# Kernel tuning notes

Measured on AMD Instinct MI355X. Metric: run time of the kernel, lower is better.

The kernel has to match this reference:

```python
import jax, jax.numpy as jnp
import numpy as np

N = 4096      # num_nodes
F = 256       # node_dim
K = 4         # num_heads
FP = 64       # out_dim per head
P_EDGE = 0.008  # edge probability (~33 avg degree)


def setup_inputs() -> dict:
    key = jax.random.key(0)
    k1, k2, k3, k4, k5 = jax.random.split(key, 5)
    x = jax.random.normal(k1, (N, F), dtype=jnp.float32)
    # binary adjacency mask with self loops so every row has a neighbor
    adj = (jax.random.uniform(k2, (N, N)) < P_EDGE).astype(jnp.float32)
    mask = jnp.maximum(adj, jnp.eye(N, dtype=jnp.float32))
    batch = jnp.zeros((N,), dtype=jnp.int32)  # unused (is_final_layer=False)
    # xavier-style init for W (node_dim -> K*FP) and attention vectors
    w_scale = np.sqrt(2.0 / (F + K * FP)).astype(np.float32)
    W = jax.random.normal(k3, (F, K * FP), dtype=jnp.float32) * w_scale
    b = jnp.zeros((K * FP,), dtype=jnp.float32)
    a_scale = np.sqrt(2.0 / (K * FP + 1)).astype(np.float32)
    a_left = jax.random.normal(k4, (1, K, FP), dtype=jnp.float32) * a_scale
    a_right = jax.random.normal(k5, (1, K, FP), dtype=jnp.float32) * a_scale
    return {"x": x, "mask": mask, "batch": batch, "W": W, "b": b,
            "a_left": a_left, "a_right": a_right}


def reference(x, mask, batch, W, b, a_left, a_right):
    # dropout prob = 0.0 (eval mode) -> identity
    x_proj = (x @ W + b).reshape(N, K, FP)                 # (N,K,F')
    score_src = (x_proj * a_left).sum(axis=-1)             # (N,K)
    score_tgt = (x_proj * a_right).sum(axis=-1)            # (N,K)
    score = score_src[:, None, :] + score_tgt[None, :, :]  # (N,N,K)
    score = jax.nn.leaky_relu(score, negative_slope=0.2)
    # non-standard global mean/std normalization (torch .std() is unbiased)
    score = (score - score.mean()) / score.std(ddof=1)
    score = jnp.exp(score)
    m = mask[:, :, None]                                   # (N,N,1)
    denom = (score * m).sum(axis=1, keepdims=True)         # (N,1,K)
    aij = (score / denom) * m                              # (N,N,K)
    attention = jnp.transpose(aij, (2, 0, 1))              # (K,N,N)
    h_prime = jnp.einsum('knm,mkf->nkf', attention, x_proj)  # (N,K,F')
    h_prime = jax.nn.elu(h_prime)
    # is_final_layer=False -> concat heads
    return h_prime.reshape(N, K * FP)
```

## Files before the change

kernel.cpp:

```cpp
#include <hip/hip_runtime.h>
#include <hip/hip_bf16.h>
#include <math.h>

#define NN 4096
#define FF 256
#define KH 4
#define FP 64
#define NCOL 256
#define MAXNBR 512
#define GEMM_BLKS 512
#define MOM_BLOCKS 1024
#define MOM_ROWS 4

__device__ __forceinline__ float bits2f(unsigned b) {
    union { unsigned u; float f; } c; c.u = b << 16; return c.f;
}
__device__ __forceinline__ int is_fp32(const void* mask) {
    return ((const unsigned*)mask)[0] == 0x3F800000u;
}

#define OFF_PART   0
#define OFF_MUSIG  65536
#define OFF_XP     131072
#define OFF_SRC    4325376
#define OFF_TGT    4390912
#define OFF_NBR    4456448
#define OFF_CNT    8650752

__global__ __launch_bounds__(256) void k_gemm_scan(
        const void* __restrict__ xr, const void* __restrict__ mask,
        const void* __restrict__ Wr, const void* __restrict__ br,
        const void* __restrict__ alr, const void* __restrict__ arr,
        float* __restrict__ xp, float* __restrict__ srcb, float* __restrict__ tgtb,
        unsigned short* __restrict__ nbr_g, int* __restrict__ cnt_g) {
    const int fl = is_fp32(mask);
    const int tid = threadIdx.x;
    __shared__ union {
        float4 xs[8][64];
        struct { unsigned short snbr[MAXNBR]; int cnt; } sc;
    } sm;

    if (blockIdx.x >= GEMM_BLKS) {
        int n = blockIdx.x - GEMM_BLKS;
        if (tid == 0) sm.sc.cnt = 0;
        __syncthreads();
        if (fl) {
            const uint4* p = (const uint4*)((const float*)mask + (size_t)n * NN);
            for (int i = tid; i < NN / 4; i += 256) {
                uint4 v = p[i]; int base = i * 4;
                if (v.x) { int s = atomicAdd(&sm.sc.cnt, 1); if (s < MAXNBR) sm.sc.snbr[s] = base + 0; }
                if (v.y) { int s = atomicAdd(&sm.sc.cnt, 1); if (s < MAXNBR) sm.sc.snbr[s] = base + 1; }
                if (v.z) { int s = atomicAdd(&sm.sc.cnt, 1); if (s < MAXNBR) sm.sc.snbr[s] = base + 2; }
                if (v.w) { int s = atomicAdd(&sm.sc.cnt, 1); if (s < MAXNBR) sm.sc.snbr[s] = base + 3; }
            }
        } else {
            const uint4* p = (const uint4*)((const unsigned short*)mask + (size_t)n * NN);
            for (int i = tid; i < NN / 8; i += 256) {
                uint4 v = p[i]; int base = i * 8;
                if (v.x & 0xFFFFu) { int s = atomicAdd(&sm.sc.cnt, 1); if (s < MAXNBR) sm.sc.snbr[s] = base + 0; }
                if (v.x >> 16)     { int s = atomicAdd(&sm.sc.cnt, 1); if (s < MAXNBR) sm.sc.snbr[s] = base + 1; }
                if (v.y & 0xFFFFu) { int s = atomicAdd(&sm.sc.cnt, 1); if (s < MAXNBR) sm.sc.snbr[s] = base + 2; }
                if (v.y >> 16)     { int s = atomicAdd(&sm.sc.cnt, 1); if (s < MAXNBR) sm.sc.snbr[s] = base + 3; }
                if (v.z & 0xFFFFu) { int s = atomicAdd(&sm.sc.cnt, 1); if (s < MAXNBR) sm.sc.snbr[s] = base + 4; }
                if (v.z >> 16)     { int s = atomicAdd(&sm.sc.cnt, 1); if (s < MAXNBR) sm.sc.snbr[s] = base + 5; }
                if (v.w & 0xFFFFu) { int s = atomicAdd(&sm.sc.cnt, 1); if (s < MAXNBR) sm.sc.snbr[s] = base + 6; }
                if (v.w >> 16)     { int s = atomicAdd(&sm.sc.cnt, 1); if (s < MAXNBR) sm.sc.snbr[s] = base + 7; }
            }
        }
        __syncthreads();
        int c = sm.sc.cnt < MAXNBR ? sm.sc.cnt : MAXNBR;
        for (int j = tid; j < c; j += 256)
            nbr_g[(size_t)n * MAXNBR + j] = sm.sc.snbr[j];
        if (tid == 0) cnt_g[n] = c;
        return;
    }

    int n0 = blockIdx.x * 8;
    if (fl) {
        const float4* xq = (const float4*)xr;
        for (int t = tid; t < 512; t += 256) {
            int r = t >> 6, q = t & 63;
            sm.xs[r][q] = xq[(size_t)(n0 + r) * 64 + q];
        }
    } else {
        const ushort4* xq = (const ushort4*)xr;
        for (int t = tid; t < 512; t += 256) {
            int r = t >> 6, q = t & 63;
            ushort4 u = xq[(size_t)(n0 + r) * 64 + q];
            float4 v; v.x = bits2f(u.x); v.y = bits2f(u.y); v.z = bits2f(u.z); v.w = bits2f(u.w);
            sm.xs[r][q] = v;
        }
    }
    __syncthreads();
    int c = tid;
    float acc[8] = {};
    if (fl) {
        const float* WF = (const float*)Wr;
        for (int kk = 0; kk < 64; ++kk) {
            float w0 = WF[(4 * kk + 0) * NCOL + c];
            float w1 = WF[(4 * kk + 1) * NCOL + c];
            float w2 = WF[(4 * kk + 2) * NCOL + c];
            float w3 = WF[(4 * kk + 3) * NCOL + c];
            #pragma unroll
            for (int r = 0; r < 8; ++r) {
                float4 xv = sm.xs[r][kk];
                acc[r] += xv.x * w0 + xv.y * w1 + xv.z * w2 + xv.w * w3;
            }
        }
    } else {
        const unsigned short* WB = (const unsigned short*)Wr;
        for (int kk = 0; kk < 64; ++kk) {
            float w0 = bits2f(WB[(4 * kk + 0) * NCOL + c]);
            float w1 = bits2f(WB[(4 * kk + 1) * NCOL + c]);
            float w2 = bits2f(WB[(4 * kk + 2) * NCOL + c]);
            float w3 = bits2f(WB[(4 * kk + 3) * NCOL + c]);
            #pragma unroll
            for (int r = 0; r < 8; ++r) {
                float4 xv = sm.xs[r][kk];
                acc[r] += xv.x * w0 + xv.y * w1 + xv.z * w2 + xv.w * w3;
            }
        }
    }
    float bv, alv, arv;
    if (fl) {
        bv  = ((const float*)br)[c];
        alv = ((const float*)alr)[c];
        arv = ((const float*)arr)[c];
    } else {
        bv  = bits2f(((const unsigned short*)br)[c]);
        alv = bits2f(((const unsigned short*)alr)[c]);
        arv = bits2f(((const unsigned short*)arr)[c]);
    }
    int wave = tid >> 6;
    int lane = tid & 63;
    #pragma unroll
    for (int r = 0; r < 8; ++r) {
        float o = acc[r] + bv;
        xp[(size_t)(n0 + r) * NCOL + c] = o;
        float sr = o * alv, tr = o * arv;
        #pragma unroll
        for (int off = 32; off; off >>= 1) {
            sr += __shfl_down(sr, off, 64);
            tr += __shfl_down(tr, off, 64);
        }
        if (lane == 0) {
            srcb[(n0 + r) * KH + wave] = sr;
            tgtb[(n0 + r) * KH + wave] = tr;
        }
    }
}

__global__ __launch_bounds__(256) void k_moments(
        const float* __restrict__ srcb, const float* __restrict__ tgtb,
        double2* __restrict__ partials) {
    const int tid = threadIdx.x;
    const int n0 = blockIdx.x * MOM_ROWS;
    const float4* s4 = (const float4*)srcb;
    float4 sv0 = s4[n0 + 0], sv1 = s4[n0 + 1], sv2 = s4[n0 + 2], sv3 = s4[n0 + 3];
    float a1_0 = 0.f, a2_0 = 0.f, a1_1 = 0.f, a2_1 = 0.f;
    float a1_2 = 0.f, a2_2 = 0.f, a1_3 = 0.f, a2_3 = 0.f;
    #pragma unroll 2
    for (int m = tid; m < NN; m += 256) {
        float4 tv = ((const float4*)tgtb)[m];
        #define MROW(sv, A1, A2) { \
            float v0 = sv.x + tv.x; v0 = fmaxf(v0, 0.2f * v0); \
            float v1 = sv.y + tv.y; v1 = fmaxf(v1, 0.2f * v1); \
            float v2 = sv.z + tv.z; v2 = fmaxf(v2, 0.2f * v2); \
            float v3 = sv.w + tv.w; v3 = fmaxf(v3, 0.2f * v3); \
            A1 += (v0 + v1) + (v2 + v3); \
            A2 += (v0 * v0 + v1 * v1) + (v2 * v2 + v3 * v3); }
        MROW(sv0, a1_0, a2_0)
        MROW(sv1, a1_1, a2_1)
        MROW(sv2, a1_2, a2_2)
        MROW(sv3, a1_3, a2_3)
        #undef MROW
    }
    __shared__ double l1[256], l2[256];
    l1[tid] = ((double)a1_0 + (double)a1_1) + ((double)a1_2 + (double)a1_3);
    l2[tid] = ((double)a2_0 + (double)a2_1) + ((double)a2_2 + (double)a2_3);
    __syncthreads();
    for (int off = 128; off; off >>= 1) {
        if (tid < off) {
            l1[tid] += l1[tid + off];
            l2[tid] += l2[tid + off];
        }
        __syncthreads();
    }
    if (tid == 0) {
        double2 pr; pr.x = l1[0]; pr.y = l2[0];
        partials[blockIdx.x] = pr;
    }
}

__global__ __launch_bounds__(256) void k_fold(
        const double2* __restrict__ partials, float* __restrict__ musig) {
    double a = 0.0, b2 = 0.0;
    for (int i = threadIdx.x; i < MOM_BLOCKS; i += 256) {
        double2 pr = partials[i];
        a += pr.x; b2 += pr.y;
    }
    __shared__ double l1[256], l2[256];
    l1[threadIdx.x] = a;
    l2[threadIdx.x] = b2;
    __syncthreads();
    for (int off = 128; off; off >>= 1) {
        if (threadIdx.x < off) {
            l1[threadIdx.x] += l1[threadIdx.x + off];
            l2[threadIdx.x] += l2[threadIdx.x + off];
        }
        __syncthreads();
    }
    if (threadIdx.x == 0) {
        double s = l1[0], ss = l2[0];
        const double tot = (double)NN * (double)NN * (double)KH;
        musig[0] = (float)(s / tot);
        musig[1] = (float)(1.0 / sqrt((ss - s * s / tot) / (tot - 1.0)));
    }
}

__global__ __launch_bounds__(256) void k_aggregate(
        const unsigned short* __restrict__ nbr_g, const int* __restrict__ cnt_g,
        const float* __restrict__ musig,
        const float* __restrict__ xp,
        const float* __restrict__ srcb, const float* __restrict__ tgtb,
        float* __restrict__ out) {
    const int tid = threadIdx.x;
    const int wave = tid >> 6, lane = tid & 63;
    __shared__ unsigned short snbr[MAXNBR];
    __shared__ float pls[MAXNBR * KH];
    __shared__ float invden[KH];
    __shared__ float4 red[4][64];
    float mu = musig[0], inv_sigma = musig[1];
    int n = blockIdx.x;
    int c = cnt_g[n];
    for (int j = tid; j < c; j += 256) snbr[j] = nbr_g[(size_t)n * MAXNBR + j];
    __syncthreads();

    for (int t = tid; t < c * KH; t += 256) {
        int j = t >> 2, k = t & 3;
        int m = snbr[j];
        float v = srcb[n * KH + k] + tgtb[m * KH + k];
        v = v > 0.f ? v : 0.2f * v;
        pls[t] = expf((v - mu) * inv_sigma);
    }
    __syncthreads();

    {
        float d = 0.f;
        for (int j = lane; j < c; j += 64) d += pls[j * KH + wave];
        #pragma unroll
        for (int off = 32; off; off >>= 1) d += __shfl_down(d, off, 64);
        if (lane == 0) invden[wave] = 1.0f / d;
    }
    __syncthreads();

    const int k = lane >> 4;
    const float4* xp4 = (const float4*)xp;
    float4 acc = make_float4(0.f, 0.f, 0.f, 0.f);
    int j = wave;
    for (; j + 4 < c; j += 8) {
        int m0 = snbr[j], m1 = snbr[j + 4];
        float w0 = pls[j * KH + k], w1 = pls[(j + 4) * KH + k];
        float4 a = xp4[(size_t)m0 * 64 + lane];
        float4 b = xp4[(size_t)m1 * 64 + lane];
        acc.x += w0 * a.x + w1 * b.x;
        acc.y += w0 * a.y + w1 * b.y;
        acc.z += w0 * a.z + w1 * b.z;
        acc.w += w0 * a.w + w1 * b.w;
    }
    if (j < c) {
        int m0 = snbr[j];
        float w0 = pls[j * KH + k];
        float4 a = xp4[(size_t)m0 * 64 + lane];
        acc.x += w0 * a.x; acc.y += w0 * a.y;
        acc.z += w0 * a.z; acc.w += w0 * a.w;
    }
    red[wave][lane] = acc;
    __syncthreads();
    if (tid < 64) {
        float4 r0 = red[0][tid], r1 = red[1][tid], r2 = red[2][tid], r3 = red[3][tid];
        float s = invden[tid >> 4];
        float4 o;
        o.x = (r0.x + r1.x + r2.x + r3.x) * s;
        o.y = (r0.y + r1.y + r2.y + r3.y) * s;
        o.z = (r0.z + r1.z + r2.z + r3.z) * s;
        o.w = (r0.w + r1.w + r2.w + r3.w) * s;
        o.x = o.x > 0.f ? o.x : expm1f(o.x);
        o.y = o.y > 0.f ? o.y : expm1f(o.y);
        o.z = o.z > 0.f ? o.z : expm1f(o.z);
        o.w = o.w > 0.f ? o.w : expm1f(o.w);
        ((float4*)out)[(size_t)n * 64 + tid] = o;
    }
}

extern "C" void kernel_launch(void* const* d_in, const int* in_sizes, int n_in,
                              void* d_out, int out_size, void* d_ws, size_t ws_size,
                              hipStream_t stream) {
    const void* x    = d_in[0];
    const void* mask = d_in[1];
    const void* W    = d_in[3];
    const void* b    = d_in[4];
    const void* al   = d_in[5];
    const void* ar   = d_in[6];

    char* ws = (char*)d_ws;
    double2* part = (double2*)(ws + OFF_PART);
    float* musig = (float*)(ws + OFF_MUSIG);
    float* xp   = (float*)(ws + OFF_XP);
    float* src  = (float*)(ws + OFF_SRC);
    float* tgt  = (float*)(ws + OFF_TGT);
    unsigned short* nbr = (unsigned short*)(ws + OFF_NBR);
    int* cntg = (int*)(ws + OFF_CNT);

    k_gemm_scan<<<GEMM_BLKS + NN, 256, 0, stream>>>(x, mask, W, b, al, ar,
                                                    xp, src, tgt, nbr, cntg);
    k_moments<<<MOM_BLOCKS, 256, 0, stream>>>(src, tgt, part);
    k_fold<<<1, 256, 0, stream>>>(part, musig);
    k_aggregate<<<NN, 256, 0, stream>>>(nbr, cntg, musig, xp, src, tgt,
                                        (float*)d_out);
}
```

Baseline: 147.4 us.

## Fuse mask scan and moment fold into aggregate kernel, drop separate launches

Moves the per-row adjacency scan out of the GEMM kernel and into the aggregate kernel, so neighbor lists are built in shared memory and no longer written to or read back from global memory. Folds the 1024 moment partials redundantly in every aggregate block, which removes the single-block fold kernel and one launch. The cost is that each of the 4096 aggregate blocks now rereads 16KB of partials and does a double-precision tree reduction, and the 64MB mask scan now sits on the critical path of the aggregate kernel instead of running alongside the GEMM.

Measured after the change: 150.6 us. 2.2% more time.

```diff
diff --git a/kernel.cpp b/kernel.cpp
--- a/kernel.cpp
+++ b/kernel.cpp
@@ -20,67 +20,25 @@
 }
 
 #define OFF_PART   0
-#define OFF_MUSIG  65536
 #define OFF_XP     131072
 #define OFF_SRC    4325376
 #define OFF_TGT    4390912
-#define OFF_NBR    4456448
-#define OFF_CNT    8650752
-
-__global__ __launch_bounds__(256) void k_gemm_scan(
+
+__global__ __launch_bounds__(256) void k_gemm(
         const void* __restrict__ xr, const void* __restrict__ mask,
         const void* __restrict__ Wr, const void* __restrict__ br,
         const void* __restrict__ alr, const void* __restrict__ arr,
-        float* __restrict__ xp, float* __restrict__ srcb, float* __restrict__ tgtb,
-        unsigned short* __restrict__ nbr_g, int* __restrict__ cnt_g) {
+        float* __restrict__ xp, float* __restrict__ srcb, float* __restrict__ tgtb) {
     const int fl = is_fp32(mask);
     const int tid = threadIdx.x;
-    __shared__ union {
-        float4 xs[8][64];
-        struct { unsigned short snbr[MAXNBR]; int cnt; } sc;
-    } sm;
-
-    if (blockIdx.x >= GEMM_BLKS) {
-        int n = blockIdx.x - GEMM_BLKS;
-        if (tid == 0) sm.sc.cnt = 0;
-        __syncthreads();
-        if (fl) {
-            const uint4* p = (const uint4*)((const float*)mask + (size_t)n * NN);
-            for (int i = tid; i < NN / 4; i += 256) {
-                uint4 v = p[i]; int base = i * 4;
-                if (v.x) { int s = atomicAdd(&sm.sc.cnt, 1); if (s < MAXNBR) sm.sc.snbr[s] = base + 0; }
-                if (v.y) { int s = atomicAdd(&sm.sc.cnt, 1); if (s < MAXNBR) sm.sc.snbr[s] = base + 1; }
-                if (v.z) { int s = atomicAdd(&sm.sc.cnt, 1); if (s < MAXNBR) sm.sc.snbr[s] = base + 2; }
-                if (v.w) { int s = atomicAdd(&sm.sc.cnt, 1); if (s < MAXNBR) sm.sc.snbr[s] = base + 3; }
-            }
-        } else {
-            const uint4* p = (const uint4*)((const unsigned short*)mask + (size_t)n * NN);
-            for (int i = tid; i < NN / 8; i += 256) {
-                uint4 v = p[i]; int base = i * 8;
-                if (v.x & 0xFFFFu) { int s = atomicAdd(&sm.sc.cnt, 1); if (s < MAXNBR) sm.sc.snbr[s] = base + 0; }
-                if (v.x >> 16)     { int s = atomicAdd(&sm.sc.cnt, 1); if (s < MAXNBR) sm.sc.snbr[s] = base + 1; }
-                if (v.y & 0xFFFFu) { int s = atomicAdd(&sm.sc.cnt, 1); if (s < MAXNBR) sm.sc.snbr[s] = base + 2; }
-                if (v.y >> 16)     { int s = atomicAdd(&sm.sc.cnt, 1); if (s < MAXNBR) sm.sc.snbr[s] = base + 3; }
-                if (v.z & 0xFFFFu) { int s = atomicAdd(&sm.sc.cnt, 1); if (s < MAXNBR) sm.sc.snbr[s] = base + 4; }
-                if (v.z >> 16)     { int s = atomicAdd(&sm.sc.cnt, 1); if (s < MAXNBR) sm.sc.snbr[s] = base + 5; }
-                if (v.w & 0xFFFFu) { int s = atomicAdd(&sm.sc.cnt, 1); if (s < MAXNBR) sm.sc.snbr[s] = base + 6; }
-                if (v.w >> 16)     { int s = atomicAdd(&sm.sc.cnt, 1); if (s < MAXNBR) sm.sc.snbr[s] = base + 7; }
-            }
-        }
-        __syncthreads();
-        int c = sm.sc.cnt < MAXNBR ? sm.sc.cnt : MAXNBR;
-        for (int j = tid; j < c; j += 256)
-            nbr_g[(size_t)n * MAXNBR + j] = sm.sc.snbr[j];
-        if (tid == 0) cnt_g[n] = c;
-        return;
-    }
+    __shared__ float4 xs[8][64];
 
     int n0 = blockIdx.x * 8;
     if (fl) {
         const float4* xq = (const float4*)xr;
         for (int t = tid; t < 512; t += 256) {
             int r = t >> 6, q = t & 63;
-            sm.xs[r][q] = xq[(size_t)(n0 + r) * 64 + q];
+            xs[r][q] = xq[(size_t)(n0 + r) * 64 + q];
         }
     } else {
         const ushort4* xq = (const ushort4*)xr;
@@ -88,7 +46,7 @@
             int r = t >> 6, q = t & 63;
             ushort4 u = xq[(size_t)(n0 + r) * 64 + q];
             float4 v; v.x = bits2f(u.x); v.y = bits2f(u.y); v.z = bits2f(u.z); v.w = bits2f(u.w);
-            sm.xs[r][q] = v;
+            xs[r][q] = v;
         }
     }
     __syncthreads();
@@ -103,7 +61,7 @@
             float w3 = WF[(4 * kk + 3) * NCOL + c];
             #pragma unroll
             for (int r = 0; r < 8; ++r) {
-                float4 xv = sm.xs[r][kk];
+                float4 xv = xs[r][kk];
                 acc[r] += xv.x * w0 + xv.y * w1 + xv.z * w2 + xv.w * w3;
             }
         }
@@ -116,7 +74,7 @@
             float w3 = bits2f(WB[(4 * kk + 3) * NCOL + c]);
             #pragma unroll
             for (int r = 0; r < 8; ++r) {
-                float4 xv = sm.xs[r][kk];
+                float4 xv = xs[r][kk];
                 acc[r] += xv.x * w0 + xv.y * w1 + xv.z * w2 + xv.w * w3;
             }
         }
@@ -192,49 +150,78 @@
     }
 }
 
-__global__ __launch_bounds__(256) void k_fold(
-        const double2* __restrict__ partials, float* __restrict__ musig) {
-    double a = 0.0, b2 = 0.0;
-    for (int i = threadIdx.x; i < MOM_BLOCKS; i += 256) {
-        double2 pr = partials[i];
-        a += pr.x; b2 += pr.y;
-    }
-    __shared__ double l1[256], l2[256];
-    l1[threadIdx.x] = a;
-    l2[threadIdx.x] = b2;
-    __syncthreads();
-    for (int off = 128; off; off >>= 1) {
-        if (threadIdx.x < off) {
-            l1[threadIdx.x] += l1[threadIdx.x + off];
-            l2[threadIdx.x] += l2[threadIdx.x + off];
-        }
-        __syncthreads();
-    }
-    if (threadIdx.x == 0) {
-        double s = l1[0], ss = l2[0];
-        const double tot = (double)NN * (double)NN * (double)KH;
-        musig[0] = (float)(s / tot);
-        musig[1] = (float)(1.0 / sqrt((ss - s * s / tot) / (tot - 1.0)));
-    }
-}
-
 __global__ __launch_bounds__(256) void k_aggregate(
-        const unsigned short* __restrict__ nbr_g, const int* __restrict__ cnt_g,
-        const float* __restrict__ musig,
+        const void* __restrict__ mask,
+        const double2* __restrict__ partials,
         const float* __restrict__ xp,
         const float* __restrict__ srcb, const float* __restrict__ tgtb,
         float* __restrict__ out) {
+    const int fl = is_fp32(mask);
     const int tid = threadIdx.x;
     const int wave = tid >> 6, lane = tid & 63;
     __shared__ unsigned short snbr[MAXNBR];
+    __shared__ int scnt;
     __shared__ float pls[MAXNBR * KH];
     __shared__ float invden[KH];
-    __shared__ float4 red[4][64];
-    float mu = musig[0], inv_sigma = musig[1];
-    int n = blockIdx.x;
-    int c = cnt_g[n];
-    for (int j = tid; j < c; j += 256) snbr[j] = nbr_g[(size_t)n * MAXNBR + j];
-    __syncthreads();
+    __shared__ float musig_s[2];
+    __shared__ union {
+        double fold[2][256];
+        float4 red[4][64];
+    } u;
+    const int n = blockIdx.x;
+    if (tid == 0) scnt = 0;
+    __syncthreads();
+
+    if (fl) {
+        const uint4* p = (const uint4*)((const float*)mask + (size_t)n * NN);
+        for (int i = tid; i < NN / 4; i += 256) {
+            uint4 v = p[i]; int base = i * 4;
+            if (v.x) { int s = atomicAdd(&scnt, 1); if (s < MAXNBR) snbr[s] = base + 0; }
+            if (v.y) { int s = atomicAdd(&scnt, 1); if (s < MAXNBR) snbr[s] = base + 1; }
+            if (v.z) { int s = atomicAdd(&scnt, 1); if (s < MAXNBR) snbr[s] = base + 2; }
+            if (v.w) { int s = atomicAdd(&scnt, 1); if (s < MAXNBR) snbr[s] = base + 3; }
+        }
+    } else {
+        const uint4* p = (const uint4*)((const unsigned short*)mask + (size_t)n * NN);
+        for (int i = tid; i < NN / 8; i += 256) {
+            uint4 v = p[i]; int base = i * 8;
+            if (v.x & 0xFFFFu) { int s = atomicAdd(&scnt, 1); if (s < MAXNBR) snbr[s] = base + 0; }
+            if (v.x >> 16)     { int s = atomicAdd(&scnt, 1); if (s < MAXNBR) snbr[s] = base + 1; }
+            if (v.y & 0xFFFFu) { int s = atomicAdd(&scnt, 1); if (s < MAXNBR) snbr[s] = base + 2; }
+            if (v.y >> 16)     { int s = atomicAdd(&scnt, 1); if (s < MAXNBR) snbr[s] = base + 3; }
+            if (v.z & 0xFFFFu) { int s = atomicAdd(&scnt, 1); if (s < MAXNBR) snbr[s] = base + 4; }
+            if (v.z >> 16)     { int s = atomicAdd(&scnt, 1); if (s < MAXNBR) snbr[s] = base + 5; }
+            if (v.w & 0xFFFFu) { int s = atomicAdd(&scnt, 1); if (s < MAXNBR) snbr[s] = base + 6; }
+            if (v.w >> 16)     { int s = atomicAdd(&scnt, 1); if (s < MAXNBR) snbr[s] = base + 7; }
+        }
+    }
+
+    {
+        double a = 0.0, b2 = 0.0;
+        for (int i = tid; i < MOM_BLOCKS; i += 256) {
+            double2 pr = partials[i];
+            a += pr.x; b2 += pr.y;
+        }
+        u.fold[0][tid] = a;
+        u.fold[1][tid] = b2;
+        __syncthreads();
+        for (int off = 128; off; off >>= 1) {
+            if (tid < off) {
+                u.fold[0][tid] += u.fold[0][tid + off];
+                u.fold[1][tid] += u.fold[1][tid + off];
+            }
+            __syncthreads();
+        }
+        if (tid == 0) {
+            double s = u.fold[0][0], ss = u.fold[1][0];
+            const double tot = (double)NN * (double)NN * (double)KH;
+            musig_s[0] = (float)(s / tot);
+            musig_s[1] = (float)(1.0 / sqrt((ss - s * s / tot) / (tot - 1.0)));
+        }
+        __syncthreads();
+    }
+    const float mu = musig_s[0], inv_sigma = musig_s[1];
+    const int c = scnt < MAXNBR ? scnt : MAXNBR;
 
     for (int t = tid; t < c * KH; t += 256) {
         int j = t >> 2, k = t & 3;
@@ -275,10 +262,10 @@
         acc.x += w0 * a.x; acc.y += w0 * a.y;
         acc.z += w0 * a.z; acc.w += w0 * a.w;
     }
-    red[wave][lane] = acc;
+    u.red[wave][lane] = acc;
     __syncthreads();
     if (tid < 64) {
-        float4 r0 = red[0][tid], r1 = red[1][tid], r2 = red[2][tid], r3 = red[3][tid];
+        float4 r0 = u.red[0][tid], r1 = u.red[1][tid], r2 = u.red[2][tid], r3 = u.red[3][tid];
         float s = invden[tid >> 4];
         float4 o;
         o.x = (r0.x + r1.x + r2.x + r3.x) * s;
@@ -305,17 +292,11 @@
 
     char* ws = (char*)d_ws;
     double2* part = (double2*)(ws + OFF_PART);
-    float* musig = (float*)(ws + OFF_MUSIG);
     float* xp   = (float*)(ws + OFF_XP);
     float* src  = (float*)(ws + OFF_SRC);
     float* tgt  = (float*)(ws + OFF_TGT);
-    unsigned short* nbr = (unsigned short*)(ws + OFF_NBR);
-    int* cntg = (int*)(ws + OFF_CNT);
-
-    k_gemm_scan<<<GEMM_BLKS + NN, 256, 0, stream>>>(x, mask, W, b, al, ar,
-                                                    xp, src, tgt, nbr, cntg);
+
+    k_gemm<<<GEMM_BLKS, 256, 0, stream>>>(x, mask, W, b, al, ar, xp, src, tgt);
     k_moments<<<MOM_BLOCKS, 256, 0, stream>>>(src, tgt, part);
-    k_fold<<<1, 256, 0, stream>>>(part, musig);
-    k_aggregate<<<NN, 256, 0, stream>>>(nbr, cntg, musig, xp, src, tgt,
-                                        (float*)d_out);
-}
+    k_aggregate<<<NN, 256, 0, stream>>>(mask, part, xp, src, tgt, (float*)d_out);
+}
```

## Compute attention scores via folded W·a vectors and fuse moments into scan/GEMM kernel

Applied to the files above, without the earlier changes.

Adds a small kernel that folds the attention vectors into W (W·a_left, W·a_right, plus bias terms) so per-node scores come directly from x without waiting on the full projection. This lets the moments reduction run in the same launch as the mask scan and the projection GEMM instead of after it, removing a dependent kernel boundary. The cost is an extra small serial kernel in front that recomputes the folded weights in every block. Summing in a different order also changes the floating-point rounding of the scores.

New measurement: 193.2 us. 1.31x slower.

```diff
diff --git a/kernel.cpp b/kernel.cpp
--- a/kernel.cpp
+++ b/kernel.cpp
@@ -8,6 +8,7 @@
 #define FP 64
 #define NCOL 256
 #define MAXNBR 512
+#define SCAN_BLKS 4096
 #define GEMM_BLKS 512
 #define MOM_BLOCKS 1024
 #define MOM_ROWS 4
@@ -27,21 +28,98 @@
 #define OFF_NBR    4456448
 #define OFF_CNT    8650752
 
-__global__ __launch_bounds__(256) void k_gemm_scan(
+__global__ __launch_bounds__(256) void k_scores(
         const void* __restrict__ xr, const void* __restrict__ mask,
         const void* __restrict__ Wr, const void* __restrict__ br,
         const void* __restrict__ alr, const void* __restrict__ arr,
-        float* __restrict__ xp, float* __restrict__ srcb, float* __restrict__ tgtb,
-        unsigned short* __restrict__ nbr_g, int* __restrict__ cnt_g) {
+        float* __restrict__ srcb, float* __restrict__ tgtb) {
+    const int fl = is_fp32(mask);
+    const int tid = threadIdx.x;
+    __shared__ float al_s[NCOL], ar_s[NCOL];
+    __shared__ float wl_s[FF][KH], wr_s[FF][KH];
+    __shared__ float bl_s[KH], brr_s[KH];
+
+    if (fl) {
+        al_s[tid] = ((const float*)alr)[tid];
+        ar_s[tid] = ((const float*)arr)[tid];
+    } else {
+        al_s[tid] = bits2f(((const unsigned short*)alr)[tid]);
+        ar_s[tid] = bits2f(((const unsigned short*)arr)[tid]);
+    }
+    __syncthreads();
+
+    if (tid < 8) {
+        int k = tid & 3, which = tid >> 2;
+        float s = 0.f;
+        for (int f = 0; f < FP; ++f) {
+            int cc = k * FP + f;
+            float bvv = fl ? ((const float*)br)[cc]
+                           : bits2f(((const unsigned short*)br)[cc]);
+            s += bvv * (which ? ar_s[cc] : al_s[cc]);
+        }
+        if (which) brr_s[k] = s; else bl_s[k] = s;
+    }
+
+    {
+        const float* WrowF = (const float*)Wr + (size_t)tid * NCOL;
+        const unsigned short* WrowB = (const unsigned short*)Wr + (size_t)tid * NCOL;
+        #pragma unroll
+        for (int k = 0; k < KH; ++k) {
+            float sl = 0.f, sr = 0.f;
+            for (int f = 0; f < FP; ++f) {
+                int cc = k * FP + f;
+                float w = fl ? WrowF[cc] : bits2f(WrowB[cc]);
+                sl += w * al_s[cc];
+                sr += w * ar_s[cc];
+            }
+            wl_s[tid][k] = sl;
+            wr_s[tid][k] = sr;
+        }
+    }
+    __syncthreads();
+
+    const int r = tid & 63, k = tid >> 6;
+    const int n = blockIdx.x * 64 + r;
+    float sl = bl_s[k], sr = brr_s[k];
+    if (fl) {
+        const float4* xrow = (const float4*)((const float*)xr + (size_t)n * FF);
+        for (int j4 = 0; j4 < FF / 4; ++j4) {
+            float4 xv = xrow[j4];
+            int j = j4 * 4;
+            sl += xv.x * wl_s[j][k] + xv.y * wl_s[j+1][k] + xv.z * wl_s[j+2][k] + xv.w * wl_s[j+3][k];
+            sr += xv.x * wr_s[j][k] + xv.y * wr_s[j+1][k] + xv.z * wr_s[j+2][k] + xv.w * wr_s[j+3][k];
+        }
+    } else {
+        const ushort4* xrow = (const ushort4*)((const unsigned short*)xr + (size_t)n * FF);
+        for (int j4 = 0; j4 < FF / 4; ++j4) {
+            ushort4 u = xrow[j4];
+            float x0 = bits2f(u.x), x1 = bits2f(u.y), x2 = bits2f(u.z), x3 = bits2f(u.w);
+            int j = j4 * 4;
+            sl += x0 * wl_s[j][k] + x1 * wl_s[j+1][k] + x2 * wl_s[j+2][k] + x3 * wl_s[j+3][k];
+            sr += x0 * wr_s[j][k] + x1 * wr_s[j+1][k] + x2 * wr_s[j+2][k] + x3 * wr_s[j+3][k];
+        }
+    }
+    srcb[n * KH + k] = sl;
+    tgtb[n * KH + k] = sr;
+}
+
+__global__ __launch_bounds__(256) void k_fused(
+        const void* __restrict__ xr, const void* __restrict__ mask,
+        const void* __restrict__ Wr, const void* __restrict__ br,
+        float* __restrict__ xp,
+        const float* __restrict__ srcb, const float* __restrict__ tgtb,
+        unsigned short* __restrict__ nbr_g, int* __restrict__ cnt_g,
+        double2* __restrict__ partials) {
     const int fl = is_fp32(mask);
     const int tid = threadIdx.x;
     __shared__ union {
         float4 xs[8][64];
         struct { unsigned short snbr[MAXNBR]; int cnt; } sc;
+        struct { double l1[256], l2[256]; } mo;
     } sm;
 
-    if (blockIdx.x >= GEMM_BLKS) {
-        int n = blockIdx.x - GEMM_BLKS;
+    if (blockIdx.x < SCAN_BLKS) {
+        int n = blockIdx.x;
         if (tid == 0) sm.sc.cnt = 0;
         __syncthreads();
         if (fl) {
@@ -75,7 +153,46 @@
         return;
     }
 
-    int n0 = blockIdx.x * 8;
+    if (blockIdx.x >= SCAN_BLKS + GEMM_BLKS) {
+        const int n0 = (blockIdx.x - SCAN_BLKS - GEMM_BLKS) * MOM_ROWS;
+        const float4* s4 = (const float4*)srcb;
+        float4 sv0 = s4[n0 + 0], sv1 = s4[n0 + 1], sv2 = s4[n0 + 2], sv3 = s4[n0 + 3];
+        float a1_0 = 0.f, a2_0 = 0.f, a1_1 = 0.f, a2_1 = 0.f;
+        float a1_2 = 0.f, a2_2 = 0.f, a1_3 = 0.f, a2_3 = 0.f;
+        #pragma unroll 2
+        for (int m = tid; m < NN; m += 256) {
+            float4 tv = ((const float4*)tgtb)[m];
+            #define MROW(sv, A1, A2) { \
+                float v0 = sv.x + tv.x; v0 = fmaxf(v0, 0.2f * v0); \
+                float v1 = sv.y + tv.y; v1 = fmaxf(v1, 0.2f * v1); \
+                float v2 = sv.z + tv.z; v2 = fmaxf(v2, 0.2f * v2); \
+                float v3 = sv.w + tv.w; v3 = fmaxf(v3, 0.2f * v3); \
+                A1 += (v0 + v1) + (v2 + v3); \
+                A2 += (v0 * v0 + v1 * v1) + (v2 * v2 + v3 * v3); }
+            MROW(sv0, a1_0, a2_0)
+            MROW(sv1, a1_1, a2_1)
+            MROW(sv2, a1_2, a2_2)
+            MROW(sv3, a1_3, a2_3)
+            #undef MROW
+        }
+        sm.mo.l1[tid] = ((double)a1_0 + (double)a1_1) + ((double)a1_2 + (double)a1_3);
+        sm.mo.l2[tid] = ((double)a2_0 + (double)a2_1) + ((double)a2_2 + (double)a2_3);
+        __syncthreads();
+        for (int off = 128; off; off >>= 1) {
+            if (tid < off) {
+                sm.mo.l1[tid] += sm.mo.l1[tid + off];
+                sm.mo.l2[tid] += sm.mo.l2[tid + off];
+            }
+            __syncthreads();
+        }
+        if (tid == 0) {
+            double2 pr; pr.x = sm.mo.l1[0]; pr.y = sm.mo.l2[0];
+            partials[blockIdx.x - SCAN_BLKS - GEMM_BLKS] = pr;
+        }
+        return;
+    }
+
+    int n0 = (blockIdx.x - SCAN_BLKS) * 8;
     if (fl) {
         const float4* xq = (const float4*)xr;
         for (int t = tid; t < 512; t += 256) {
@@ -121,75 +238,10 @@
             }
         }
     }
-    float bv, alv, arv;
-    if (fl) {
-        bv  = ((const float*)br)[c];
-        alv = ((const float*)alr)[c];
-        arv = ((const float*)arr)[c];
-    } else {
-        bv  = bits2f(((const unsigned short*)br)[c]);
-        alv = bits2f(((const unsigned short*)alr)[c]);
-        arv = bits2f(((const unsigned short*)arr)[c]);
-    }
-    int wave = tid >> 6;
-    int lane = tid & 63;
+    float bv = fl ? ((const float*)br)[c] : bits2f(((const unsigned short*)br)[c]);
     #pragma unroll
-    for (int r = 0; r < 8; ++r) {
-        float o = acc[r] + bv;
-        xp[(size_t)(n0 + r) * NCOL + c] = o;
-        float sr = o * alv, tr = o * arv;
-        #pragma unroll
-        for (int off = 32; off; off >>= 1) {
-            sr += __shfl_down(sr, off, 64);
-            tr += __shfl_down(tr, off, 64);
-        }
-        if (lane == 0) {
-            srcb[(n0 + r) * KH + wave] = sr;
-            tgtb[(n0 + r) * KH + wave] = tr;
-        }
-    }
-}
-
-__global__ __launch_bounds__(256) void k_moments(
-        const float* __restrict__ srcb, const float* __restrict__ tgtb,
-        double2* __restrict__ partials) {
-    const int tid = threadIdx.x;
-    const int n0 = blockIdx.x * MOM_ROWS;
-    const float4* s4 = (const float4*)srcb;
-    float4 sv0 = s4[n0 + 0], sv1 = s4[n0 + 1], sv2 = s4[n0 + 2], sv3 = s4[n0 + 3];
-    float a1_0 = 0.f, a2_0 = 0.f, a1_1 = 0.f, a2_1 = 0.f;
-    float a1_2 = 0.f, a2_2 = 0.f, a1_3 = 0.f, a2_3 = 0.f;
-    #pragma unroll 2
-    for (int m = tid; m < NN; m += 256) {
-        float4 tv = ((const float4*)tgtb)[m];
-        #define MROW(sv, A1, A2) { \
-            float v0 = sv.x + tv.x; v0 = fmaxf(v0, 0.2f * v0); \
-            float v1 = sv.y + tv.y; v1 = fmaxf(v1, 0.2f * v1); \
-            float v2 = sv.z + tv.z; v2 = fmaxf(v2, 0.2f * v2); \
-            float v3 = sv.w + tv.w; v3 = fmaxf(v3, 0.2f * v3); \
-            A1 += (v0 + v1) + (v2 + v3); \
-            A2 += (v0 * v0 + v1 * v1) + (v2 * v2 + v3 * v3); }
-        MROW(sv0, a1_0, a2_0)
-        MROW(sv1, a1_1, a2_1)
-        MROW(sv2, a1_2, a2_2)
-        MROW(sv3, a1_3, a2_3)
-        #undef MROW
-    }
-    __shared__ double l1[256], l2[256];
-    l1[tid] = ((double)a1_0 + (double)a1_1) + ((double)a1_2 + (double)a1_3);
-    l2[tid] = ((double)a2_0 + (double)a2_1) + ((double)a2_2 + (double)a2_3);
-    __syncthreads();
-    for (int off = 128; off; off >>= 1) {
-        if (tid < off) {
-            l1[tid] += l1[tid + off];
-            l2[tid] += l2[tid + off];
-        }
-        __syncthreads();
-    }
-    if (tid == 0) {
-        double2 pr; pr.x = l1[0]; pr.y = l2[0];
-        partials[blockIdx.x] = pr;
-    }
+    for (int r = 0; r < 8; ++r)
+        xp[(size_t)(n0 + r) * NCOL + c] = acc[r] + bv;
 }
 
 __global__ __launch_bounds__(256) void k_fold(
@@ -312,9 +364,9 @@
     unsigned short* nbr = (unsigned short*)(ws + OFF_NBR);
     int* cntg = (int*)(ws + OFF_CNT);
 
-    k_gemm_scan<<<GEMM_BLKS + NN, 256, 0, stream>>>(x, mask, W, b, al, ar,
-                                                    xp, src, tgt, nbr, cntg);
-    k_moments<<<MOM_BLOCKS, 256, 0, stream>>>(src, tgt, part);
+    k_scores<<<64, 256, 0, stream>>>(x, mask, W, b, al, ar, src, tgt);
+    k_fused<<<SCAN_BLKS + GEMM_BLKS + MOM_BLOCKS, 256, 0, stream>>>(
+        x, mask, W, b, xp, src, tgt, nbr, cntg, part);
     k_fold<<<1, 256, 0, stream>>>(part, musig);
     k_aggregate<<<NN, 256, 0, stream>>>(nbr, cntg, musig, xp, src, tgt,
                                         (float*)d_out);
```
